# Kernel optimization log

Hardware: AMD Instinct MI355X
Metric: run time of the kernel (lower is better)

Reference implementation:

```python
import jax, jax.numpy as jnp
import numpy as np
import math

NUM_HEAD = 4
GROUPS = 32
EPS = 1e-5


def setup_inputs() -> dict:
    key = jax.random.key(0)
    k1, k2, k3 = jax.random.split(key, 3)
    B, C, H, W = 2, 256, 64, 64
    x = jax.random.normal(k1, (B, C, H, W), dtype=jnp.float32)
    gn_w = jnp.ones((C,), dtype=jnp.float32)
    gn_b = jnp.zeros((C,), dtype=jnp.float32)
    # scaling_init 'u' with scale=1: bound = sqrt(3*2/(fan_in+fan_out))
    fan = (C + 3 * C) / 2
    bound_qkv = math.sqrt(3.0 / fan)
    qkv_w = jax.random.uniform(k2, (3 * C, C), dtype=jnp.float32, minval=-bound_qkv, maxval=bound_qkv)
    bound_o = math.sqrt(3e-10 / C)
    o_w = jax.random.uniform(k3, (C, C), dtype=jnp.float32, minval=-bound_o, maxval=bound_o)
    o_b = jnp.zeros((C,), dtype=jnp.float32)
    return {"x": x, "gn_w": gn_w, "gn_b": gn_b, "qkv_w": qkv_w, "o_w": o_w, "o_b": o_b}


def _group_norm(x, w, b):
    B, C, H, W = x.shape
    xg = x.reshape(B, GROUPS, C // GROUPS, H, W)
    mean = xg.mean(axis=(2, 3, 4), keepdims=True)
    var = xg.var(axis=(2, 3, 4), keepdims=True)
    xn = ((xg - mean) * jax.lax.rsqrt(var + EPS)).reshape(B, C, H, W)
    return xn * w[None, :, None, None] + b[None, :, None, None]


def reference(x, gn_w, gn_b, qkv_w, o_w, o_b):
    B, C, H, W = x.shape
    hd = C // NUM_HEAD
    S = H * W
    norm = _group_norm(x, gn_w, gn_b)
    # 1x1 conv (no bias) == channel matmul
    qkv = jnp.einsum('oc,bchw->bohw', qkv_w, norm)
    qkv = qkv.reshape(B, NUM_HEAD, 3 * hd, S)
    q, k, v = jnp.split(qkv, 3, axis=2)  # each [B, nh, hd, S]
    scale = 1.0 / math.sqrt(C)  # note: sqrt(C), not sqrt(head_dim), per source
    attn = jnp.einsum('bncs,bnct->bnst', q, k) * scale  # [B, nh, S, S]
    attn = jax.nn.softmax(attn, axis=-1)
    out = jnp.einsum('bnst,bnct->bncs', attn, v).reshape(B, C, H, W)
    out = jnp.einsum('oc,bchw->bohw', o_w, out) + o_b[None, :, None, None]
    return out + x
```

## Files before the change

kernel.cpp:

```cpp
#include <hip/hip_runtime.h>
#include <hip/hip_bf16.h>

typedef __hip_bfloat16 bf16;
typedef short short8 __attribute__((ext_vector_type(8)));
typedef float f32x4 __attribute__((ext_vector_type(4)));

__device__ __forceinline__ float b2f(bf16 v) { return __bfloat162float(v); }

__device__ __forceinline__ unsigned short f2bf(float x) {
  unsigned u = __builtin_bit_cast(unsigned, x);
  unsigned r = u + 0x7fffu + ((u >> 16) & 1u);
  return (unsigned short)(r >> 16);
}
__device__ __forceinline__ unsigned pk2(float a, float b) {
  return (unsigned)f2bf(a) | ((unsigned)f2bf(b) << 16);
}
__device__ __forceinline__ unsigned pk2t(float a, float b) {
  return __builtin_amdgcn_perm(__builtin_bit_cast(unsigned, b),
                               __builtin_bit_cast(unsigned, a), 0x07060302u);
}
__device__ __forceinline__ float rd(const void* p, size_t i, int is32) {
  return is32 ? ((const float*)p)[i] : b2f(((const bf16*)p)[i]);
}
__device__ __forceinline__ float blo(unsigned w) {
  return __builtin_bit_cast(float, w << 16);
}
__device__ __forceinline__ float bhi(unsigned w) {
  return __builtin_bit_cast(float, w & 0xffff0000u);
}
__device__ __forceinline__ float fexp2(float x) {
  return __builtin_amdgcn_exp2f(x);
}

#define CQ 0.09016844005556022f

__global__ void __launch_bounds__(256) detect_kernel(const void* __restrict__ x,
                                                     int* __restrict__ flag) {
  __shared__ int cnt[256];
  const bf16* xb = (const bf16*)x;
  int c = 0;
  for (int i = threadIdx.x; i < 4096; i += 256) {
    float v = fabsf(b2f(xb[2 * i]));
    if (v >= 0.0009765625f && v <= 1024.0f) c++;
  }
  cnt[threadIdx.x] = c;
  __syncthreads();
  for (int off = 128; off > 0; off >>= 1) {
    if (threadIdx.x < off) cnt[threadIdx.x] += cnt[threadIdx.x + off];
    __syncthreads();
  }
  if (threadIdx.x == 0) *flag = (cnt[0] < 2048) ? 1 : 0;
}

__global__ void __launch_bounds__(256) pre1_kernel(
    const void* __restrict__ x, const void* __restrict__ gn_w,
    const void* __restrict__ gn_b, const int* __restrict__ flag,
    float* __restrict__ scale, float* __restrict__ shift,
    short* __restrict__ xT) {
  __shared__ __align__(16) float F[64][72];
  const int t = threadIdx.x;
  const int is32 = *flag;
  if (blockIdx.x < 512) {
    const int bx = blockIdx.x;
    const int b = bx >> 8, rest = bx & 255;
    const int s0 = (rest >> 2) * 64, c0 = (rest & 3) * 64;
    if (is32) {
      const float* xp = (const float*)x;
#pragma unroll
      for (int k = 0; k < 4; k++) {
        int idx = k * 256 + t, cl = idx >> 4, c4 = idx & 15;
        float4 v = *(const float4*)&xp[(size_t)(b * 256 + c0 + cl) * 4096 + s0 +
                                       c4 * 4];
        *(float4*)&F[cl][c4 * 4] = v;
      }
    } else {
      const bf16* xp = (const bf16*)x;
#pragma unroll
      for (int k = 0; k < 2; k++) {
        int idx = k * 256 + t, cl = idx >> 3, c8 = idx & 7;
        uint4 u = *(const uint4*)&xp[(size_t)(b * 256 + c0 + cl) * 4096 + s0 +
                                     c8 * 8];
        float4 f0, f1;
        f0.x = blo(u.x); f0.y = bhi(u.x); f0.z = blo(u.y); f0.w = bhi(u.y);
        f1.x = blo(u.z); f1.y = bhi(u.z); f1.z = blo(u.w); f1.w = bhi(u.w);
        *(float4*)&F[cl][c8 * 8] = f0;
        *(float4*)&F[cl][c8 * 8 + 4] = f1;
      }
    }
    __syncthreads();
#pragma unroll
    for (int k = 0; k < 8; k++) {
      int idx = k * 256 + t;
      int sl = idx >> 5, c2 = (idx & 31) * 2;
      unsigned u = pk2(F[c2][sl], F[c2 + 1][sl]);
      *(unsigned*)&xT[((size_t)b * 4096 + s0 + sl) * 256 + c0 + c2] = u;
    }
  } else {
    const int idx0 = blockIdx.x - 512;
    const int b = idx0 >> 5, g = idx0 & 31;
    const size_t base = (size_t)(b * 256 + g * 8) * 4096;
    float s = 0.f, ss = 0.f;
    if (is32) {
      const float4* p = (const float4*)((const float*)x + base);
      for (int i = t; i < 8192; i += 256) {
        float4 v = p[i];
        s += (v.x + v.y) + (v.z + v.w);
        ss += v.x * v.x + v.y * v.y + v.z * v.z + v.w * v.w;
      }
    } else {
      const uint4* p = (const uint4*)((const bf16*)x + base);
      for (int i = t; i < 4096; i += 256) {
        uint4 u = p[i];
#pragma unroll
        for (int k = 0; k < 4; k++) {
          unsigned w = (&u.x)[k];
          float lo = blo(w), hi = bhi(w);
          s += lo + hi;
          ss += lo * lo + hi * hi;
        }
      }
    }
    float* rs = &F[0][0];
    float* rq = rs + 256;
    rs[t] = s;
    rq[t] = ss;
    __syncthreads();
    for (int off = 128; off > 0; off >>= 1) {
      if (t < off) {
        rs[t] += rs[t + off];
        rq[t] += rq[t + off];
      }
      __syncthreads();
    }
    if (t < 8) {
      const float inv_n = 1.f / 32768.f;
      float mean = rs[0] * inv_n;
      float var = rq[0] * inv_n - mean * mean;
      float rstd = rsqrtf(var + 1e-5f);
      int c = g * 8 + t;
      float sc = rd(gn_w, c, is32) * rstd;
      scale[b * 256 + c] = sc;
      shift[b * 256 + c] = rd(gn_b, c, is32) - mean * sc;
    }
  }
}

__global__ void __launch_bounds__(256) pre2_kernel(
    const void* __restrict__ qkv_w, const void* __restrict__ o_w,
    const void* __restrict__ o_b, const float* __restrict__ scale,
    const float* __restrict__ shift, const int* __restrict__ flag,
    short* __restrict__ W2, float* __restrict__ bias2, short* __restrict__ owb,
    float* __restrict__ obf) {
  const int is32 = *flag;
  if (blockIdx.x < 192) {
    const int b = blockIdx.y;
    const int o = blockIdx.x * 4 + (threadIdx.x >> 6);
    const int lane = threadIdx.x & 63;
    const float f = (o % 192 < 64) ? CQ : 1.0f;
    float w[4], acc = 0.f;
#pragma unroll
    for (int k = 0; k < 4; k++) {
      int c = lane * 4 + k;
      w[k] = rd(qkv_w, (size_t)o * 256 + c, is32);
      acc += w[k] * shift[b * 256 + c];
      w[k] = w[k] * scale[b * 256 + c] * f;
    }
#pragma unroll
    for (int m = 1; m < 64; m <<= 1) acc += __shfl_xor(acc, m);
    if (lane == 0) bias2[b * 768 + o] = acc * f;
    uint2 u;
    u.x = pk2(w[0], w[1]);
    u.y = pk2(w[2], w[3]);
    *(uint2*)&W2[((size_t)b * 768 + o) * 256 + lane * 4] = u;
  } else if (blockIdx.y == 0) {
    int bx = blockIdx.x - 192;
    int i = (bx * 256 + threadIdx.x) * 4;
    uint2 u;
    u.x = pk2(rd(o_w, i, is32), rd(o_w, i + 1, is32));
    u.y = pk2(rd(o_w, i + 2, is32), rd(o_w, i + 3, is32));
    *(uint2*)&owb[i] = u;
    if (bx == 0) obf[threadIdx.x] = rd(o_b, threadIdx.x, is32);
  }
}

__global__ void __launch_bounds__(256) gemm_qkv_kernel(
    const short* __restrict__ xT, const short* __restrict__ W2,
    const float* __restrict__ bias2, short* __restrict__ qT,
    short* __restrict__ kF, short* __restrict__ vF) {
  __shared__ __align__(16) short lds[128 * 72 + 64 * 72];
  short* At = lds;
  short* Bt = lds + 128 * 72;
  const int t = threadIdx.x;
  const int wave = t >> 6, lane = t & 63;
  const int ln = lane & 15, quad = lane >> 4;
  const int s0 = blockIdx.x * 128, by = blockIdx.y, b = blockIdx.z;
  const int o0 = by * 64;
  const short* xg = xT + ((size_t)b * 4096 + s0) * 256;
  const short* wg = W2 + ((size_t)b * 768 + o0) * 256;

  f32x4 acc[2][4];
#pragma unroll
  for (int mt = 0; mt < 2; mt++)
#pragma unroll
    for (int nt = 0; nt < 4; nt++) {
      f32x4 z = {0.f, 0.f, 0.f, 0.f};
      acc[mt][nt] = z;
    }

  for (int kt = 0; kt < 4; kt++) {
    __syncthreads();
    {
      int r = t >> 1, ch = t & 1;
#pragma unroll
      for (int j = 0; j < 4; j++)
        *(uint4*)&At[r * 72 + ch * 32 + j * 8] =
            *(const uint4*)&xg[(size_t)r * 256 + kt * 64 + ch * 32 + j * 8];
    }
    {
      int r = t >> 2, cq = t & 3;
#pragma unroll
      for (int j = 0; j < 2; j++)
        *(uint4*)&Bt[r * 72 + cq * 16 + j * 8] =
            *(const uint4*)&wg[(size_t)r * 256 + kt * 64 + cq * 16 + j * 8];
    }
    __syncthreads();
#pragma unroll
    for (int kd = 0; kd < 2; kd++) {
      short8 a[2], bb[4];
#pragma unroll
      for (int mt = 0; mt < 2; mt++)
        a[mt] = *(const short8*)&At[(wave * 32 + mt * 16 + ln) * 72 + kd * 32 +
                                    quad * 8];
#pragma unroll
      for (int nt = 0; nt < 4; nt++)
        bb[nt] = *(const short8*)&Bt[(nt * 16 + ln) * 72 + kd * 32 + quad * 8];
#pragma unroll
      for (int mt = 0; mt < 2; mt++)
#pragma unroll
        for (int nt = 0; nt < 4; nt++)
          acc[mt][nt] = __builtin_amdgcn_mfma_f32_16x16x32_bf16(
              a[mt], bb[nt], acc[mt][nt], 0, 0, 0);
    }
  }

  const int h = by / 3, seg = by % 3;
  const size_t bh = (size_t)b * 4 + h;
  __syncthreads();
  if (seg != 2) {
    short* T = At;
#pragma unroll
    for (int mt = 0; mt < 2; mt++)
#pragma unroll
      for (int nt = 0; nt < 4; nt++)
#pragma unroll
        for (int r = 0; r < 4; r++)
          T[(wave * 32 + mt * 16 + quad * 4 + r) * 72 + nt * 16 + ln] =
              (short)f2bf(acc[mt][nt][r] + bias2[b * 768 + o0 + nt * 16 + ln]);
    __syncthreads();
    if (seg == 0) {
      short* dst = qT + (bh * 4096 + s0) * 64;
      int r = t >> 1, ch = t & 1;
#pragma unroll
      for (int j = 0; j < 2; j++)
        *(uint4*)&dst[r * 64 + ch * 32 + j * 8] =
            *(const uint4*)&T[r * 72 + ch * 32 + j * 8];
    } else {
      short* dstf = kF + bh * 262144;
#pragma unroll
      for (int c = 0; c < 4; c++) {
        int cid = wave * 4 + c;
        int tile = cid >> 1, kd = cid & 1;
        short8 v =
            *(const short8*)&T[(tile * 16 + ln) * 72 + kd * 32 + quad * 8];
        *(short8*)&dstf[(size_t)((s0 / 16 + tile) * 2 + kd) * 512 + lane * 8] =
            v;
      }
    }
  } else {
    short* T2 = At;
#pragma unroll
    for (int mt = 0; mt < 2; mt++)
#pragma unroll
      for (int nt = 0; nt < 4; nt++) {
        float bv = bias2[b * 768 + o0 + nt * 16 + ln];
        uint2 u;
        u.x = pk2(acc[mt][nt][0] + bv, acc[mt][nt][1] + bv);
        u.y = pk2(acc[mt][nt][2] + bv, acc[mt][nt][3] + bv);
        *(uint2*)&T2[(nt * 16 + ln) * 132 + wave * 32 + mt * 16 + quad * 4] = u;
      }
    __syncthreads();
    short* dstf = vF + bh * 262144;
#pragma unroll
    for (int c = 0; c < 4; c++) {
      int cid = wave * 4 + c;
      int ktl = cid >> 3, rem = cid & 7, dt = rem >> 1, kc = rem & 1;
      short8 v = *(const short8*)&T2[(dt * 16 + ln) * 132 + ktl * 64 + kc * 32 +
                                     quad * 8];
      *(short8*)&dstf[(size_t)(((s0 / 64 + ktl) * 4 + dt) * 2 + kc) * 512 +
                      lane * 8] = v;
    }
  }
}

__global__ void __launch_bounds__(256, 2) flash_kernel(
    const short* __restrict__ qT, const short* __restrict__ kF,
    const short* __restrict__ vF, short* __restrict__ attT) {
  __shared__ float smem[4 * 64 * 34];
  const int t = threadIdx.x;
  const int wave = t >> 6, lane = t & 63;
  const int ln = lane & 15, quad = lane >> 4;
  const int L = blockIdx.x;
  const int bh = L & 7;
  const int b = bh >> 2, h = bh & 3;
  const int q0 = (L >> 3) * 32;

  const short* qg = qT + ((size_t)bh * 4096 + q0) * 64;
  const short* kf = kF + (size_t)bh * 262144;
  const short* vf = vF + (size_t)bh * 262144;

  short8 qf[2][2];
#pragma unroll
  for (int qt = 0; qt < 2; qt++)
#pragma unroll
    for (int kd = 0; kd < 2; kd++)
      qf[qt][kd] =
          *(const short8*)&qg[(qt * 16 + ln) * 64 + kd * 32 + quad * 8];

  f32x4 ot[2][4];
#pragma unroll
  for (int qt = 0; qt < 2; qt++)
#pragma unroll
    for (int dt = 0; dt < 4; dt++) {
      f32x4 z = {0.f, 0.f, 0.f, 0.f};
      ot[qt][dt] = z;
    }
  float lres[2] = {0.f, 0.f};

  auto LOADKV = [&](short8(&ka)[4][2], short8(&va)[4][2], int it) {
    const short* kb = kf + (size_t)(wave * 64 + it * 4) * 1024;
#pragma unroll
    for (int ct = 0; ct < 4; ct++)
#pragma unroll
      for (int kd = 0; kd < 2; kd++)
        ka[ct][kd] = *(const short8*)&kb[(ct * 2 + kd) * 512 + lane * 8];
    const short* vb = vf + (size_t)(wave * 16 + it) * 4096;
#pragma unroll
    for (int dt = 0; dt < 4; dt++)
#pragma unroll
      for (int kc = 0; kc < 2; kc++)
        va[dt][kc] = *(const short8*)&vb[(dt * 2 + kc) * 512 + lane * 8];
  };

  auto STEP = [&](const short8(&ka)[4][2], const short8(&va)[4][2]) {
    f32x4 st[2][4];
#pragma unroll
    for (int qt = 0; qt < 2; qt++)
#pragma unroll
      for (int ct = 0; ct < 4; ct++) {
        f32x4 z = {0.f, 0.f, 0.f, 0.f};
        st[qt][ct] = z;
      }
#pragma unroll
    for (int kd = 0; kd < 2; kd++)
#pragma unroll
      for (int ct = 0; ct < 4; ct++) {
        st[0][ct] = __builtin_amdgcn_mfma_f32_16x16x32_bf16(
            ka[ct][kd], qf[0][kd], st[0][ct], 0, 0, 0);
        st[1][ct] = __builtin_amdgcn_mfma_f32_16x16x32_bf16(
            ka[ct][kd], qf[1][kd], st[1][ct], 0, 0, 0);
      }
    unsigned pk[2][4][2];
#pragma unroll
    for (int qt = 0; qt < 2; qt++) {
      float sum = 0.f;
#pragma unroll
      for (int ct = 0; ct < 4; ct++) {
        float p0 = fexp2(st[qt][ct][0]);
        float p1 = fexp2(st[qt][ct][1]);
        float p2 = fexp2(st[qt][ct][2]);
        float p3 = fexp2(st[qt][ct][3]);
        sum += (p0 + p1) + (p2 + p3);
        pk[qt][ct][0] = pk2t(p0, p1);
        pk[qt][ct][1] = pk2t(p2, p3);
      }
      lres[qt] += sum;
    }
#pragma unroll
    for (int kc = 0; kc < 2; kc++) {
      const int tt = kc * 2 + (quad >> 1);
      const int qs = (quad & 1) * 2;
#pragma unroll
      for (int qt = 0; qt < 2; qt++) {
        union {
          unsigned u[4];
          short8 s;
        } bu;
        bu.u[0] = (unsigned)__shfl((int)pk[qt][tt][0], qs * 16 + ln);
        bu.u[1] = (unsigned)__shfl((int)pk[qt][tt][1], qs * 16 + ln);
        bu.u[2] = (unsigned)__shfl((int)pk[qt][tt][0], (qs + 1) * 16 + ln);
        bu.u[3] = (unsigned)__shfl((int)pk[qt][tt][1], (qs + 1) * 16 + ln);
#pragma unroll
        for (int dt = 0; dt < 4; dt++)
          ot[qt][dt] = __builtin_amdgcn_mfma_f32_16x16x32_bf16(
              va[dt][kc], bu.s, ot[qt][dt], 0, 0, 0);
      }
    }
  };

  short8 kaA[4][2], vaA[4][2], kaB[4][2], vaB[4][2];
  LOADKV(kaA, vaA, 0);
#pragma unroll 1
  for (int it = 0; it < 16; it += 2) {
    LOADKV(kaB, vaB, it + 1);
    STEP(kaA, vaA);
    if (it < 14) LOADKV(kaA, vaA, it + 2);
    STEP(kaB, vaB);
  }

#pragma unroll
  for (int qt = 0; qt < 2; qt++) {
    lres[qt] += __shfl_xor(lres[qt], 16);
    lres[qt] += __shfl_xor(lres[qt], 32);
  }
  float* my = smem + (wave * 64 + lane) * 34;
#pragma unroll
  for (int qt = 0; qt < 2; qt++) {
#pragma unroll
    for (int dt = 0; dt < 4; dt++)
      *(f32x4*)&my[qt * 16 + dt * 4] = ot[qt][dt];
    my[32 + qt] = lres[qt];
  }
  __syncthreads();

#pragma unroll
  for (int qt = 0; qt < 2; qt++) {
    float lf = 0.f;
    f32x4 of = {0.f, 0.f, 0.f, 0.f};
#pragma unroll
    for (int w = 0; w < 4; w++) {
      const float* pw = smem + (w * 64 + lane) * 34;
      lf += pw[32 + qt];
      f32x4 o = *(const f32x4*)&pw[qt * 16 + wave * 4];
#pragma unroll
      for (int r = 0; r < 4; r++) of[r] += o[r];
    }
    float invl = 1.f / lf;
    int s = q0 + qt * 16 + ln;
    short* ap =
        attT + ((size_t)b * 4096 + s) * 256 + h * 64 + wave * 16 + quad * 4;
    uint2 u;
    u.x = pk2(of[0] * invl, of[1] * invl);
    u.y = pk2(of[2] * invl, of[3] * invl);
    *(uint2*)ap = u;
  }
}

__global__ void __launch_bounds__(256) gemm_o_kernel(
    const short* __restrict__ owb, const short* __restrict__ attT,
    const float* __restrict__ obf, const void* __restrict__ xres,
    void* __restrict__ out, const int* __restrict__ flag) {
  __shared__ __align__(16) float ldsf[64 * 66];
  short* Bt = (short*)ldsf;
  short* At = Bt + 64 * 72;
  const int t = threadIdx.x;
  const int wave = t >> 6, lane = t & 63;
  const int ln = lane & 15, quad = lane >> 4;
  const int s0 = blockIdx.x * 64, o0 = blockIdx.y * 64, b = blockIdx.z;
  const short* ag = attT + ((size_t)b * 4096 + s0) * 256;

  f32x4 acc[4];
#pragma unroll
  for (int mt = 0; mt < 4; mt++) {
    f32x4 z = {0.f, 0.f, 0.f, 0.f};
    acc[mt] = z;
  }

  for (int kt = 0; kt < 4; kt++) {
    __syncthreads();
    {
      int r = t >> 2, cq = t & 3;
#pragma unroll
      for (int j = 0; j < 2; j++)
        *(uint4*)&Bt[r * 72 + cq * 16 + j * 8] =
            *(const uint4*)&ag[(size_t)r * 256 + kt * 64 + cq * 16 + j * 8];
    }
    {
      int r = t >> 2, cq = t & 3;
#pragma unroll
      for (int j = 0; j < 2; j++)
        *(uint4*)&At[r * 72 + cq * 16 + j * 8] =
            *(const uint4*)&owb[(size_t)(o0 + r) * 256 + kt * 64 + cq * 16 +
                                j * 8];
    }
    __syncthreads();
#pragma unroll
    for (int kd = 0; kd < 2; kd++) {
      short8 a[4];
#pragma unroll
      for (int mt = 0; mt < 4; mt++)
        a[mt] = *(const short8*)&At[(mt * 16 + ln) * 72 + kd * 32 + quad * 8];
      short8 bb =
          *(const short8*)&Bt[(wave * 16 + ln) * 72 + kd * 32 + quad * 8];
#pragma unroll
      for (int mt = 0; mt < 4; mt++)
        acc[mt] =
            __builtin_amdgcn_mfma_f32_16x16x32_bf16(a[mt], bb, acc[mt], 0, 0, 0);
    }
  }

  __syncthreads();
#pragma unroll
  for (int mt = 0; mt < 4; mt++)
#pragma unroll
    for (int r = 0; r < 4; r++)
      ldsf[(mt * 16 + quad * 4 + r) * 66 + wave * 16 + ln] = acc[mt][r];
  __syncthreads();

  const int is32 = *flag;
#pragma unroll
  for (int j = 0; j < 4; j++) {
    int ol = j * 16 + (t >> 4);
    int sl = (t & 15) * 4;
    f32x4 v = *(const f32x4*)&ldsf[ol * 66 + sl];
    int o = o0 + ol;
    float bv = obf[o];
    size_t base = ((size_t)b * 256 + o) * 4096 + s0 + sl;
    if (is32) {
      const float4 rr = *(const float4*)&((const float*)xres)[base];
      float4 w;
      w.x = v[0] + bv + rr.x;
      w.y = v[1] + bv + rr.y;
      w.z = v[2] + bv + rr.z;
      w.w = v[3] + bv + rr.w;
      *(float4*)&((float*)out)[base] = w;
    } else {
      const uint2 rr = *(const uint2*)&((const bf16*)xres)[base];
      uint2 w;
      w.x = pk2(v[0] + bv + blo(rr.x), v[1] + bv + bhi(rr.x));
      w.y = pk2(v[2] + bv + blo(rr.y), v[3] + bv + bhi(rr.y));
      *(uint2*)&((bf16*)out)[base] = w;
    }
  }
}

extern "C" void kernel_launch(void* const* d_in, const int* in_sizes, int n_in,
                              void* d_out, int out_size, void* d_ws,
                              size_t ws_size, hipStream_t stream) {
  float* ws = (float*)d_ws;
  int* flag = (int*)ws;
  float* scale = ws + 256;
  float* shift = ws + 768;
  float* bias2 = ws + 1280;
  float* obf = ws + 2816;
  short* owb = (short*)(ws + 3072);
  short* W2 = (short*)(ws + 35840);
  short* xT = (short*)(ws + 232448);
  short* qT = (short*)(ws + 1281024);
  short* kF = (short*)(ws + 2329600);
  short* vF = (short*)(ws + 3378176);
  short* attT = (short*)(ws + 4426752);

  detect_kernel<<<1, 256, 0, stream>>>(d_in[0], flag);
  pre1_kernel<<<576, 256, 0, stream>>>(d_in[0], d_in[1], d_in[2], flag, scale,
                                       shift, xT);
  pre2_kernel<<<dim3(256, 2), 256, 0, stream>>>(d_in[3], d_in[4], d_in[5],
                                                scale, shift, flag, W2, bias2,
                                                owb, obf);
  gemm_qkv_kernel<<<dim3(32, 12, 2), 256, 0, stream>>>(xT, W2, bias2, qT, kF,
                                                       vF);
  flash_kernel<<<1024, 256, 0, stream>>>(qT, kF, vF, attT);
  gemm_o_kernel<<<dim3(64, 4, 2), 256, 0, stream>>>(owb, attT, obf, d_in[0],
                                                    d_out, flag);
}
```

Before: 185.0 us.

## Shrink flash attention block to 16 queries and 32-key steps for higher occupancy

Each flash block now handles 16 query rows instead of 32, and each inner step covers 32 keys instead of 64. The grid doubles to 2048 blocks and launch bounds rise to 4 blocks per CU. Per-thread register and LDS footprint drops, aiming for more resident waves to hide K/V load latency. The cost is that each K/V tile is reused by half as many queries, so global and L2 traffic for K/V doubles.

```diff
diff --git a/kernel.cpp b/kernel.cpp
--- a/kernel.cpp
+++ b/kernel.cpp
@@ -302,150 +302,120 @@
   }
 }
 
-__global__ void __launch_bounds__(256, 2) flash_kernel(
+__global__ void __launch_bounds__(256, 4) flash_kernel(
     const short* __restrict__ qT, const short* __restrict__ kF,
     const short* __restrict__ vF, short* __restrict__ attT) {
-  __shared__ float smem[4 * 64 * 34];
+  __shared__ float smem[4 * 64 * 20];
   const int t = threadIdx.x;
   const int wave = t >> 6, lane = t & 63;
   const int ln = lane & 15, quad = lane >> 4;
   const int L = blockIdx.x;
   const int bh = L & 7;
   const int b = bh >> 2, h = bh & 3;
-  const int q0 = (L >> 3) * 32;
+  const int q0 = (L >> 3) * 16;
 
   const short* qg = qT + ((size_t)bh * 4096 + q0) * 64;
-  const short* kf = kF + (size_t)bh * 262144;
-  const short* vf = vF + (size_t)bh * 262144;
-
-  short8 qf[2][2];
-#pragma unroll
-  for (int qt = 0; qt < 2; qt++)
-#pragma unroll
-    for (int kd = 0; kd < 2; kd++)
-      qf[qt][kd] =
-          *(const short8*)&qg[(qt * 16 + ln) * 64 + kd * 32 + quad * 8];
-
-  f32x4 ot[2][4];
-#pragma unroll
-  for (int qt = 0; qt < 2; qt++)
-#pragma unroll
-    for (int dt = 0; dt < 4; dt++) {
-      f32x4 z = {0.f, 0.f, 0.f, 0.f};
-      ot[qt][dt] = z;
-    }
-  float lres[2] = {0.f, 0.f};
-
-  auto LOADKV = [&](short8(&ka)[4][2], short8(&va)[4][2], int it) {
-    const short* kb = kf + (size_t)(wave * 64 + it * 4) * 1024;
-#pragma unroll
-    for (int ct = 0; ct < 4; ct++)
+  const short* kf = kF + (size_t)bh * 262144 + (size_t)wave * 65536;
+  const short* vf = vF + (size_t)bh * 262144 + (size_t)wave * 65536;
+
+  short8 qf[2];
+#pragma unroll
+  for (int kd = 0; kd < 2; kd++)
+    qf[kd] = *(const short8*)&qg[ln * 64 + kd * 32 + quad * 8];
+
+  f32x4 ot[4];
+#pragma unroll
+  for (int dt = 0; dt < 4; dt++) {
+    f32x4 z = {0.f, 0.f, 0.f, 0.f};
+    ot[dt] = z;
+  }
+  float lres = 0.f;
+
+  auto LOADKV = [&](short8(&ka)[2][2], short8(&va)[4], int it) {
+    const short* kb = kf + (size_t)(it * 2) * 1024;
+#pragma unroll
+    for (int ct = 0; ct < 2; ct++)
 #pragma unroll
       for (int kd = 0; kd < 2; kd++)
         ka[ct][kd] = *(const short8*)&kb[(ct * 2 + kd) * 512 + lane * 8];
-    const short* vb = vf + (size_t)(wave * 16 + it) * 4096;
+    const short* vb = vf + (size_t)(it >> 1) * 4096;
+    const int kc = it & 1;
 #pragma unroll
     for (int dt = 0; dt < 4; dt++)
-#pragma unroll
-      for (int kc = 0; kc < 2; kc++)
-        va[dt][kc] = *(const short8*)&vb[(dt * 2 + kc) * 512 + lane * 8];
+      va[dt] = *(const short8*)&vb[(dt * 2 + kc) * 512 + lane * 8];
   };
 
-  auto STEP = [&](const short8(&ka)[4][2], const short8(&va)[4][2]) {
-    f32x4 st[2][4];
-#pragma unroll
-    for (int qt = 0; qt < 2; qt++)
-#pragma unroll
-      for (int ct = 0; ct < 4; ct++) {
-        f32x4 z = {0.f, 0.f, 0.f, 0.f};
-        st[qt][ct] = z;
-      }
+  auto STEP = [&](const short8(&ka)[2][2], const short8(&va)[4]) {
+    f32x4 st[2];
+#pragma unroll
+    for (int ct = 0; ct < 2; ct++) {
+      f32x4 z = {0.f, 0.f, 0.f, 0.f};
+      st[ct] = z;
+    }
 #pragma unroll
     for (int kd = 0; kd < 2; kd++)
 #pragma unroll
-      for (int ct = 0; ct < 4; ct++) {
-        st[0][ct] = __builtin_amdgcn_mfma_f32_16x16x32_bf16(
-            ka[ct][kd], qf[0][kd], st[0][ct], 0, 0, 0);
-        st[1][ct] = __builtin_amdgcn_mfma_f32_16x16x32_bf16(
-            ka[ct][kd], qf[1][kd], st[1][ct], 0, 0, 0);
-      }
-    unsigned pk[2][4][2];
-#pragma unroll
-    for (int qt = 0; qt < 2; qt++) {
-      float sum = 0.f;
-#pragma unroll
-      for (int ct = 0; ct < 4; ct++) {
-        float p0 = fexp2(st[qt][ct][0]);
-        float p1 = fexp2(st[qt][ct][1]);
-        float p2 = fexp2(st[qt][ct][2]);
-        float p3 = fexp2(st[qt][ct][3]);
-        sum += (p0 + p1) + (p2 + p3);
-        pk[qt][ct][0] = pk2t(p0, p1);
-        pk[qt][ct][1] = pk2t(p2, p3);
-      }
-      lres[qt] += sum;
-    }
-#pragma unroll
-    for (int kc = 0; kc < 2; kc++) {
-      const int tt = kc * 2 + (quad >> 1);
-      const int qs = (quad & 1) * 2;
-#pragma unroll
-      for (int qt = 0; qt < 2; qt++) {
-        union {
-          unsigned u[4];
-          short8 s;
-        } bu;
-        bu.u[0] = (unsigned)__shfl((int)pk[qt][tt][0], qs * 16 + ln);
-        bu.u[1] = (unsigned)__shfl((int)pk[qt][tt][1], qs * 16 + ln);
-        bu.u[2] = (unsigned)__shfl((int)pk[qt][tt][0], (qs + 1) * 16 + ln);
-        bu.u[3] = (unsigned)__shfl((int)pk[qt][tt][1], (qs + 1) * 16 + ln);
-#pragma unroll
-        for (int dt = 0; dt < 4; dt++)
-          ot[qt][dt] = __builtin_amdgcn_mfma_f32_16x16x32_bf16(
-              va[dt][kc], bu.s, ot[qt][dt], 0, 0, 0);
-      }
-    }
+      for (int ct = 0; ct < 2; ct++)
+        st[ct] = __builtin_amdgcn_mfma_f32_16x16x32_bf16(ka[ct][kd], qf[kd],
+                                                         st[ct], 0, 0, 0);
+    unsigned pk[2][2];
+#pragma unroll
+    for (int ct = 0; ct < 2; ct++) {
+      float p0 = fexp2(st[ct][0]);
+      float p1 = fexp2(st[ct][1]);
+      float p2 = fexp2(st[ct][2]);
+      float p3 = fexp2(st[ct][3]);
+      lres += (p0 + p1) + (p2 + p3);
+      pk[ct][0] = pk2t(p0, p1);
+      pk[ct][1] = pk2t(p2, p3);
+    }
+    const int tt = quad >> 1;
+    const int qs = (quad & 1) * 2;
+    union {
+      unsigned u[4];
+      short8 s;
+    } bu;
+    bu.u[0] = (unsigned)__shfl((int)pk[tt][0], qs * 16 + ln);
+    bu.u[1] = (unsigned)__shfl((int)pk[tt][1], qs * 16 + ln);
+    bu.u[2] = (unsigned)__shfl((int)pk[tt][0], (qs + 1) * 16 + ln);
+    bu.u[3] = (unsigned)__shfl((int)pk[tt][1], (qs + 1) * 16 + ln);
+#pragma unroll
+    for (int dt = 0; dt < 4; dt++)
+      ot[dt] = __builtin_amdgcn_mfma_f32_16x16x32_bf16(va[dt], bu.s, ot[dt], 0,
+                                                       0, 0);
   };
 
-  short8 kaA[4][2], vaA[4][2], kaB[4][2], vaB[4][2];
+  short8 kaA[2][2], vaA[4], kaB[2][2], vaB[4];
   LOADKV(kaA, vaA, 0);
 #pragma unroll 1
-  for (int it = 0; it < 16; it += 2) {
+  for (int it = 0; it < 32; it += 2) {
     LOADKV(kaB, vaB, it + 1);
     STEP(kaA, vaA);
-    if (it < 14) LOADKV(kaA, vaA, it + 2);
+    if (it < 30) LOADKV(kaA, vaA, it + 2);
     STEP(kaB, vaB);
   }
 
-#pragma unroll
-  for (int qt = 0; qt < 2; qt++) {
-    lres[qt] += __shfl_xor(lres[qt], 16);
-    lres[qt] += __shfl_xor(lres[qt], 32);
-  }
-  float* my = smem + (wave * 64 + lane) * 34;
-#pragma unroll
-  for (int qt = 0; qt < 2; qt++) {
-#pragma unroll
-    for (int dt = 0; dt < 4; dt++)
-      *(f32x4*)&my[qt * 16 + dt * 4] = ot[qt][dt];
-    my[32 + qt] = lres[qt];
-  }
+  lres += __shfl_xor(lres, 16);
+  lres += __shfl_xor(lres, 32);
+  float* my = smem + (wave * 64 + lane) * 20;
+#pragma unroll
+  for (int dt = 0; dt < 4; dt++) *(f32x4*)&my[dt * 4] = ot[dt];
+  my[16] = lres;
   __syncthreads();
 
-#pragma unroll
-  for (int qt = 0; qt < 2; qt++) {
+  {
     float lf = 0.f;
     f32x4 of = {0.f, 0.f, 0.f, 0.f};
 #pragma unroll
     for (int w = 0; w < 4; w++) {
-      const float* pw = smem + (w * 64 + lane) * 34;
-      lf += pw[32 + qt];
-      f32x4 o = *(const f32x4*)&pw[qt * 16 + wave * 4];
+      const float* pw = smem + (w * 64 + lane) * 20;
+      lf += pw[16];
+      f32x4 o = *(const f32x4*)&pw[wave * 4];
 #pragma unroll
       for (int r = 0; r < 4; r++) of[r] += o[r];
     }
     float invl = 1.f / lf;
-    int s = q0 + qt * 16 + ln;
+    int s = q0 + ln;
     short* ap =
         attT + ((size_t)b * 4096 + s) * 256 + h * 64 + wave * 16 + quad * 4;
     uint2 u;
@@ -503,8 +473,8 @@
           *(const short8*)&Bt[(wave * 16 + ln) * 72 + kd * 32 + quad * 8];
 #pragma unroll
       for (int mt = 0; mt < 4; mt++)
-        acc[mt] =
-            __builtin_amdgcn_mfma_f32_16x16x32_bf16(a[mt], bb, acc[mt], 0, 0, 0);
+        acc[mt] = __builtin_amdgcn_mfma_f32_16x16x32_bf16(a[mt], bb, acc[mt],
+                                                          0, 0, 0);
     }
   }
 
@@ -568,7 +538,7 @@
                                                 owb, obf);
   gemm_qkv_kernel<<<dim3(32, 12, 2), 256, 0, stream>>>(xT, W2, bias2, qT, kF,
                                                        vF);
-  flash_kernel<<<1024, 256, 0, stream>>>(qT, kF, vF, attT);
+  flash_kernel<<<2048, 256, 0, stream>>>(qT, kF, vF, attT);
   gemm_o_kernel<<<dim3(64, 4, 2), 256, 0, stream>>>(owb, attT, obf, d_in[0],
                                                     d_out, flag);
 }
```

Result: faster. 175.9 us, median of 2 (-4.9%).
